# Performance work log

Measured on AMD Instinct MI355X. Metric: run time of the kernel, lower is better.

The kernel has to match this reference:

```python
import jax, jax.numpy as jnp
import numpy as np

N, H, W = 2, 64, 64
HM, WM = 2 * H - 1, 2 * W - 1


def setup_inputs() -> dict:
    key = jax.random.key(0)
    x = jax.random.normal(key, (N, HM * WM, H, W), dtype=jnp.float32)
    return {"x": x}


def reference(x):
    n, c, h_feat, w_feat = x.shape
    hm, wm = 2 * h_feat - 1, 2 * w_feat - 1
    xr = x.reshape(n, hm, wm, h_feat, w_feat)
    xt = jnp.transpose(xr, (0, 3, 4, 1, 2))
    hh = jnp.arange(h_feat)
    ww = jnp.arange(w_feat)
    idxh = hh[None, :] - hh[:, None] + (h_feat - 1)
    idxw = ww[None, :] - ww[:, None] + (w_feat - 1)
    a = jnp.take_along_axis(xt, idxh[None, :, None, :, None], axis=3)
    out = jnp.take_along_axis(a, idxw[None, None, :, None, :], axis=4)
    return out.reshape(n, h_feat * w_feat, h_feat, w_feat)
```

## Files before the change

kernel.cpp:

```cpp
#include <hip/hip_runtime.h>


#define PSA_H 64
#define PSA_W 64
#define PSA_HM 127
#define PSA_WM 127
#define PSA_HW (PSA_H * PSA_W)
#define PSA_CHW (PSA_HM * PSA_WM)

__global__ __launch_bounds__(256) void psa_distribute_kernel(
    const float* __restrict__ in, float* __restrict__ out) {
    __shared__ float lds[PSA_W * PSA_W];

    const int b = blockIdx.x;
    const int n = b >> 12;
    const int h = (b >> 6) & 63;
    const int i = b & 63;
    const int di = i - h + (PSA_H - 1);

    const size_t in_base =
        ((size_t)n * PSA_CHW + (size_t)di * PSA_WM) * (size_t)PSA_HW
        + (size_t)h * PSA_W;

    const int lane = threadIdx.x & 63;
    const int wv   = threadIdx.x >> 6;
    const int rr   = lane >> 4;
    const int wl   = lane & 15;
    const int wbase = wl << 2;

#pragma unroll
    for (int g4 = 0; g4 < 8; ++g4) {
        const int g  = g4 * 4 + wv;
        const int dj = g * 4 + rr;
        const bool active = (dj < PSA_WM) &&
                            (wbase + 3 >= PSA_W - 1 - dj) &&
                            (wbase <= 2 * (PSA_W - 1) - dj);
        if (active) {
            const float4 v =
                *(const float4*)(in + in_base + (size_t)dj * PSA_HW + wbase);
            const int jb = dj + wbase - (PSA_W - 1);
#pragma unroll
            for (int e = 0; e < 4; ++e) {
                const int j = jb + e;
                if ((unsigned)j < (unsigned)PSA_W) {
                    lds[(wbase + e) * PSA_W + j] = ((const float*)&v)[e];
                }
            }
        }
    }
    __syncthreads();

    const size_t out_base =
        ((size_t)(n * PSA_HW) + (size_t)h * PSA_W) * (size_t)PSA_HW
        + (size_t)i * PSA_W;

    const float4* lds4 = (const float4*)lds;
    float4* out4 = (float4*)(out + out_base);
    const int t = threadIdx.x;
#pragma unroll
    for (int k = 0; k < 4; ++k) {
        const int id = k * 256 + t;
        const int w  = id >> 4;
        const int j4 = id & 15;
        out4[w * (PSA_HW / 4) + j4] = lds4[id];
    }
}

extern "C" void kernel_launch(void* const* d_in, const int* in_sizes, int n_in,
                              void* d_out, int out_size, void* d_ws, size_t ws_size,
                              hipStream_t stream) {
    const float* x = (const float*)d_in[0];
    float* out = (float*)d_out;
    const int nblocks = 2 * PSA_H * PSA_H;
    psa_distribute_kernel<<<nblocks, 256, 0, stream>>>(x, out);
}
```

Measured before the change: 73.23 us.

## Process four (h,i) pairs per block with XCD-aware block remapping

```diff
diff --git a/kernel.cpp b/kernel.cpp
--- a/kernel.cpp
+++ b/kernel.cpp
@@ -7,62 +7,73 @@
 #define PSA_WM 127
 #define PSA_HW (PSA_H * PSA_W)
 #define PSA_CHW (PSA_HM * PSA_WM)
+#define NPAIR 4
 
-__global__ __launch_bounds__(256) void psa_distribute_kernel(
+__global__ __launch_bounds__(512) void psa_distribute_kernel(
     const float* __restrict__ in, float* __restrict__ out) {
-    __shared__ float lds[PSA_W * PSA_W];
+    __shared__ float lds[NPAIR * PSA_HW];
 
-    const int b = blockIdx.x;
-    const int n = b >> 12;
-    const int h = (b >> 6) & 63;
-    const int i = b & 63;
-    const int di = i - h + (PSA_H - 1);
+    const int b   = blockIdx.x;
+    const int xcd = b & 7;
+    const int s   = (xcd << 8) + (b >> 3);
+    const int n   = s >> 10;
+    const int u   = (s >> 4) & 63;
+    const int h0  = (s & 15) << 2;
 
-    const size_t in_base =
-        ((size_t)n * PSA_CHW + (size_t)di * PSA_WM) * (size_t)PSA_HW
-        + (size_t)h * PSA_W;
+    size_t in_base[NPAIR];
+    size_t out_base[NPAIR];
+#pragma unroll
+    for (int p = 0; p < NPAIR; ++p) {
+        const int h  = h0 + p;
+        const int i  = (h + u) & 63;
+        const int di = i - h + (PSA_H - 1);
+        in_base[p]  = ((size_t)n * PSA_CHW + (size_t)di * PSA_WM) * PSA_HW
+                      + (size_t)h * PSA_W;
+        out_base[p] = ((size_t)n * PSA_HW + (size_t)h * PSA_W) * PSA_HW
+                      + (size_t)i * PSA_W;
+    }
 
-    const int lane = threadIdx.x & 63;
-    const int wv   = threadIdx.x >> 6;
-    const int rr   = lane >> 4;
-    const int wl   = lane & 15;
+    const int t     = threadIdx.x;
+    const int wl    = t & 15;
+    const int djo   = (t >> 4) & 3;
+    const int wv    = t >> 6;
     const int wbase = wl << 2;
 
 #pragma unroll
-    for (int g4 = 0; g4 < 8; ++g4) {
-        const int g  = g4 * 4 + wv;
-        const int dj = g * 4 + rr;
-        const bool active = (dj < PSA_WM) &&
+    for (int it = 0; it < 4; ++it) {
+        const int dj = it * 32 + wv * 4 + djo;
+        const bool row_ok = (dj < PSA_WM) &&
                             (wbase + 3 >= PSA_W - 1 - dj) &&
                             (wbase <= 2 * (PSA_W - 1) - dj);
-        if (active) {
-            const float4 v =
-                *(const float4*)(in + in_base + (size_t)dj * PSA_HW + wbase);
+        if (row_ok) {
             const int jb = dj + wbase - (PSA_W - 1);
 #pragma unroll
-            for (int e = 0; e < 4; ++e) {
-                const int j = jb + e;
-                if ((unsigned)j < (unsigned)PSA_W) {
-                    lds[(wbase + e) * PSA_W + j] = ((const float*)&v)[e];
+            for (int p = 0; p < NPAIR; ++p) {
+                const float4 v = *(const float4*)(
+                    in + in_base[p] + (size_t)dj * PSA_HW + wbase);
+#pragma unroll
+                for (int e = 0; e < 4; ++e) {
+                    const int j = jb + e;
+                    if ((unsigned)j < (unsigned)PSA_W) {
+                        lds[p * PSA_HW + (wbase + e) * PSA_W + j] =
+                            ((const float*)&v)[e];
+                    }
                 }
             }
         }
     }
     __syncthreads();
 
-    const size_t out_base =
-        ((size_t)(n * PSA_HW) + (size_t)h * PSA_W) * (size_t)PSA_HW
-        + (size_t)i * PSA_W;
-
     const float4* lds4 = (const float4*)lds;
-    float4* out4 = (float4*)(out + out_base);
-    const int t = threadIdx.x;
 #pragma unroll
-    for (int k = 0; k < 4; ++k) {
-        const int id = k * 256 + t;
-        const int w  = id >> 4;
-        const int j4 = id & 15;
-        out4[w * (PSA_HW / 4) + j4] = lds4[id];
+    for (int it = 0; it < 8; ++it) {
+        const int idx = it * 512 + t;
+        const int p   = idx >> 10;
+        const int rem = idx & 1023;
+        const int w   = rem >> 4;
+        const int j4  = rem & 15;
+        float4* dst = (float4*)(out + out_base[p]);
+        dst[w * (PSA_HW / 4) + j4] = lds4[idx];
     }
 }
 
@@ -71,6 +82,6 @@
                               hipStream_t stream) {
     const float* x = (const float*)d_in[0];
     float* out = (float*)d_out;
-    const int nblocks = 2 * PSA_H * PSA_H;
-    psa_distribute_kernel<<<nblocks, 256, 0, stream>>>(x, out);
+    const int nblocks = 2 * PSA_H * PSA_H / NPAIR;
+    psa_distribute_kernel<<<nblocks, 512, 0, stream>>>(x, out);
 }
```

Result: slower. 81.95 us (+11.9%).
